# Kernel optimization log

Hardware: AMD Instinct MI355X
Metric: run time of the kernel (lower is better)

The kernel has to match this reference:

```python
import jax, jax.numpy as jnp
import numpy as np

H = 256
VOCAB = 32000
B = 128
T = 2048


def setup_inputs() -> dict:
    key = jax.random.key(0)
    ks = jax.random.split(key, 14)
    s = 0.05
    return {
        "tokens": jax.random.randint(ks[0], (B, 1), 0, VOCAB),
        "hidden": jax.random.normal(ks[1], (1, B, H), jnp.float32),
        "encoder_outputs": jax.random.normal(ks[2], (T, B, H), jnp.float32),
        "emb_table": jax.random.normal(ks[3], (VOCAB + 1, H), jnp.float32) * s,
        "attn_W": jax.random.normal(ks[4], (1, 2 * H), jnp.float32) * s,
        "attn_b": jax.random.normal(ks[5], (1,), jnp.float32) * s,
        "comb_W": jax.random.normal(ks[6], (H, 2 * H), jnp.float32) * s,
        "comb_b": jax.random.normal(ks[7], (H,), jnp.float32) * s,
        "gru_Wih": jax.random.normal(ks[8], (3 * H, H), jnp.float32) * s,
        "gru_Whh": jax.random.normal(ks[9], (3 * H, H), jnp.float32) * s,
        "gru_bih": jax.random.normal(ks[10], (3 * H,), jnp.float32) * s,
        "gru_bhh": jax.random.normal(ks[11], (3 * H,), jnp.float32) * s,
        "out_W": jax.random.normal(ks[12], (VOCAB, H), jnp.float32) * s,
        "out_b": jax.random.normal(ks[13], (VOCAB,), jnp.float32) * s,
    }


def reference(tokens, hidden, encoder_outputs, emb_table, attn_W, attn_b,
              comb_W, comb_b, gru_Wih, gru_Whh, gru_bih, gru_bhh, out_W, out_b):
    h = hidden.shape[-1]
    # Embedding lookup: [B,1] -> [B,1,H] -> [1,B,H]
    emb = jnp.transpose(emb_table[tokens], (1, 0, 2))
    # Additive attention: Linear([hidden; enc_t]) -> scalar score per position.
    # attn_W splits into hidden part (first H cols) and encoder part (last H).
    W_h, W_e = attn_W[:, :h], attn_W[:, h:]          # [1,H] each
    scores = (jnp.einsum('tbh,oh->tbo', encoder_outputs, W_e)
              + jnp.einsum('lbh,oh->lbo', hidden, W_h)  # broadcast over T
              + attn_b)                                  # [T,B,1]
    attn_w = jax.nn.softmax(scores, axis=0)              # softmax over time
    # Context: weighted sum over time -> [1,B,H]
    ctx = jnp.einsum('tbo,tbh->obh', attn_w, encoder_outputs)
    # Combine embedded input with context, relu
    x = jnp.concatenate([emb, ctx], axis=2)              # [1,B,2H]
    x = jax.nn.relu(jnp.einsum('lbk,hk->lbh', x, comb_W) + comb_b)  # [1,B,H]
    # Single GRU step (PyTorch gate ordering: r, z, n)
    gx = x[0] @ gru_Wih.T + gru_bih                      # [B,3H]
    gh = hidden[0] @ gru_Whh.T + gru_bhh                 # [B,3H]
    r = jax.nn.sigmoid(gx[:, :h] + gh[:, :h])
    z = jax.nn.sigmoid(gx[:, h:2 * h] + gh[:, h:2 * h])
    n = jnp.tanh(gx[:, 2 * h:] + r * gh[:, 2 * h:])
    h_new = ((1.0 - z) * n + z * hidden[0])[None]        # [1,B,H]
    # Output projection + log_softmax over vocab
    logits = jnp.einsum('lbh,vh->lbv', h_new, out_W) + out_b
    logp = jax.nn.log_softmax(logits, axis=2)            # [1,B,V]
    return (logp, h_new, jnp.transpose(attn_w, (1, 0, 2)), ctx)
```

## Files before the change

### kernel.cpp

```cpp
#include <hip/hip_runtime.h>
#include <cstddef>

constexpr int H  = 256;
constexpr int Bb = 128;
constexpr int T  = 2048;
constexpr int V  = 32000;
constexpr int SPLITS = 16;
constexpr int TC = T / SPLITS;

__global__ __launch_bounds__(256) void k_attn(
    const float* __restrict__ enc, const float* __restrict__ hidden,
    const float* __restrict__ attn_W, const float* __restrict__ attn_b,
    float* __restrict__ scores, float* __restrict__ ctx_part) {
  const int b = blockIdx.y, chunk = blockIdx.x, tid = threadIdx.x;
  const int lane = tid & 63, wave = tid >> 6;
  __shared__ float red[16];
  __shared__ float hb_sh;

  const float we = attn_W[H + tid];
  const float wh = attn_W[tid];
  const float hv = hidden[b * H + tid];

  float p = wh * hv;
  #pragma unroll
  for (int off = 32; off; off >>= 1) p += __shfl_down(p, off);
  if (lane == 0) red[wave] = p;
  __syncthreads();
  if (tid == 0) hb_sh = red[0] + red[1] + red[2] + red[3] + attn_b[0];
  __syncthreads();
  const float hb = hb_sh;

  float acc = 0.f;
  const float* encb = enc + (size_t)chunk * TC * (Bb * H) + (size_t)b * H + tid;
  const int t0base = chunk * TC;

  for (int t = 0; t < TC; t += 4) {
    float e0 = encb[(size_t)(t + 0) * (Bb * H)];
    float e1 = encb[(size_t)(t + 1) * (Bb * H)];
    float e2 = encb[(size_t)(t + 2) * (Bb * H)];
    float e3 = encb[(size_t)(t + 3) * (Bb * H)];
    float p0 = e0 * we, p1 = e1 * we, p2 = e2 * we, p3 = e3 * we;
    #pragma unroll
    for (int off = 32; off; off >>= 1) {
      p0 += __shfl_down(p0, off);
      p1 += __shfl_down(p1, off);
      p2 += __shfl_down(p2, off);
      p3 += __shfl_down(p3, off);
    }
    __syncthreads();
    if (lane == 0) {
      red[wave * 4 + 0] = p0; red[wave * 4 + 1] = p1;
      red[wave * 4 + 2] = p2; red[wave * 4 + 3] = p3;
    }
    __syncthreads();
    float s0 = red[0] + red[4] + red[8]  + red[12] + hb;
    float s1 = red[1] + red[5] + red[9]  + red[13] + hb;
    float s2 = red[2] + red[6] + red[10] + red[14] + hb;
    float s3 = red[3] + red[7] + red[11] + red[15] + hb;
    float w0 = __expf(s0), w1 = __expf(s1), w2 = __expf(s2), w3 = __expf(s3);
    acc += w0 * e0 + w1 * e1 + w2 * e2 + w3 * e3;
    if (tid < 4) {
      float sv = (tid == 0) ? s0 : (tid == 1) ? s1 : (tid == 2) ? s2 : s3;
      scores[(size_t)b * T + t0base + t + tid] = sv;
    }
  }
  ctx_part[((size_t)b * SPLITS + chunk) * H + tid] = acc;
}

__global__ __launch_bounds__(256) void k_softmax_ctx(
    const float* __restrict__ scores, const float* __restrict__ ctx_part,
    float* __restrict__ attn_o, float* __restrict__ ctx_o) {
  const int b = blockIdx.x, tid = threadIdx.x;
  const int lane = tid & 63, wave = tid >> 6;
  __shared__ float red[4];
  __shared__ float m_sh, l_sh;

  const float* sb = scores + (size_t)b * T;
  float s[8];
  #pragma unroll
  for (int q = 0; q < 8; q++) s[q] = sb[tid + 256 * q];

  float mx = s[0];
  #pragma unroll
  for (int q = 1; q < 8; q++) mx = fmaxf(mx, s[q]);
  #pragma unroll
  for (int off = 32; off; off >>= 1) mx = fmaxf(mx, __shfl_down(mx, off));
  if (lane == 0) red[wave] = mx;
  __syncthreads();
  if (tid == 0) m_sh = fmaxf(fmaxf(red[0], red[1]), fmaxf(red[2], red[3]));
  __syncthreads();
  const float m = m_sh;

  float w[8];
  float ps = 0.f;
  #pragma unroll
  for (int q = 0; q < 8; q++) { w[q] = __expf(s[q] - m); ps += w[q]; }
  #pragma unroll
  for (int off = 32; off; off >>= 1) ps += __shfl_down(ps, off);
  __syncthreads();
  if (lane == 0) red[wave] = ps;
  __syncthreads();
  if (tid == 0) l_sh = red[0] + red[1] + red[2] + red[3];
  __syncthreads();
  const float inv = 1.f / l_sh;

  #pragma unroll
  for (int q = 0; q < 8; q++) attn_o[(size_t)b * T + tid + 256 * q] = w[q] * inv;

  float c = 0.f;
  #pragma unroll
  for (int si = 0; si < SPLITS; si++) c += ctx_part[((size_t)b * SPLITS + si) * H + tid];
  ctx_o[(size_t)b * H + tid] = c * __expf(-m) * inv;
}

__global__ __launch_bounds__(256) void k_comb_gru(
    const int* __restrict__ tokens, const float* __restrict__ hidden,
    const float* __restrict__ emb_table,
    const float* __restrict__ comb_W, const float* __restrict__ comb_b,
    const float* __restrict__ Wih, const float* __restrict__ Whh,
    const float* __restrict__ bih, const float* __restrict__ bhh,
    const float* __restrict__ ctx_o, float* __restrict__ hnew) {
  const int b = blockIdx.x, tid = threadIdx.x;
  __shared__ __align__(16) float x2[2 * H];
  __shared__ __align__(16) float hid[H];
  __shared__ __align__(16) float xs[H];

  const int tok = tokens[b];
  x2[tid]     = emb_table[(size_t)tok * H + tid];
  x2[H + tid] = ctx_o[(size_t)b * H + tid];
  hid[tid]    = hidden[(size_t)b * H + tid];
  __syncthreads();

  {
    const float4* wr = (const float4*)(comb_W + (size_t)tid * (2 * H));
    const float4* xr = (const float4*)x2;
    float a = 0.f;
    #pragma unroll 8
    for (int k = 0; k < (2 * H) / 4; k++) {
      float4 w = wr[k], x = xr[k];
      a += w.x * x.x + w.y * x.y + w.z * x.z + w.w * x.w;
    }
    a += comb_b[tid];
    xs[tid] = fmaxf(a, 0.f);
  }
  __syncthreads();

  auto dot256 = [](const float* __restrict__ row, const float* __restrict__ v) -> float {
    const float4* r4 = (const float4*)row;
    const float4* v4 = (const float4*)v;
    float a = 0.f;
    #pragma unroll 8
    for (int k = 0; k < H / 4; k++) {
      float4 w = r4[k], x = v4[k];
      a += w.x * x.x + w.y * x.y + w.z * x.z + w.w * x.w;
    }
    return a;
  };

  float gxr = dot256(Wih + (size_t)tid * H,             xs) + bih[tid];
  float gxz = dot256(Wih + (size_t)(tid + H) * H,       xs) + bih[tid + H];
  float gxn = dot256(Wih + (size_t)(tid + 2 * H) * H,   xs) + bih[tid + 2 * H];
  float ghr = dot256(Whh + (size_t)tid * H,             hid) + bhh[tid];
  float ghz = dot256(Whh + (size_t)(tid + H) * H,       hid) + bhh[tid + H];
  float ghn = dot256(Whh + (size_t)(tid + 2 * H) * H,   hid) + bhh[tid + 2 * H];

  float r = 1.f / (1.f + __expf(-(gxr + ghr)));
  float z = 1.f / (1.f + __expf(-(gxz + ghz)));
  float n = tanhf(gxn + r * ghn);
  hnew[(size_t)b * H + tid] = (1.f - z) * n + z * hid[tid];
}

__global__ __launch_bounds__(256) void k_logits(
    const float* __restrict__ hnew, const float* __restrict__ out_W,
    const float* __restrict__ out_b, float* __restrict__ logits) {
  const int tid = threadIdx.x;
  const int v0 = blockIdx.x * 128;
  const int tx = tid & 15, ty = tid >> 4;
  __shared__ __align__(16) float lW[128][36];
  __shared__ __align__(16) float lH[128][36];

  float acc[8][8];
  #pragma unroll
  for (int i = 0; i < 8; i++)
    #pragma unroll
    for (int j = 0; j < 8; j++) acc[i][j] = 0.f;

  for (int k0 = 0; k0 < H; k0 += 32) {
    #pragma unroll
    for (int q = 0; q < 4; q++) {
      int idx = q * 1024 + tid * 4;
      int r = idx >> 5, c = idx & 31;
      float4 wv = *(const float4*)(out_W + (size_t)(v0 + r) * H + k0 + c);
      *(float4*)(&lW[r][c]) = wv;
      float4 hv = *(const float4*)(hnew + (size_t)r * H + k0 + c);
      *(float4*)(&lH[r][c]) = hv;
    }
    __syncthreads();
    #pragma unroll 4
    for (int kk = 0; kk < 32; kk++) {
      float hreg[8], wreg[8];
      #pragma unroll
      for (int i = 0; i < 8; i++) hreg[i] = lH[ty + 16 * i][kk];
      #pragma unroll
      for (int j = 0; j < 8; j++) wreg[j] = lW[tx + 16 * j][kk];
      #pragma unroll
      for (int i = 0; i < 8; i++)
        #pragma unroll
        for (int j = 0; j < 8; j++)
          acc[i][j] = fmaf(hreg[i], wreg[j], acc[i][j]);
    }
    __syncthreads();
  }

  float bj[8];
  #pragma unroll
  for (int j = 0; j < 8; j++) bj[j] = out_b[v0 + tx + 16 * j];
  #pragma unroll
  for (int i = 0; i < 8; i++) {
    int b = ty + 16 * i;
    float* dst = logits + (size_t)b * V + v0 + tx;
    #pragma unroll
    for (int j = 0; j < 8; j++) dst[16 * j] = acc[i][j] + bj[j];
  }
}

__global__ __launch_bounds__(256) void k_lse(
    const float* __restrict__ logits, float* __restrict__ lse) {
  const int b = blockIdx.x, tid = threadIdx.x;
  const int lane = tid & 63, wave = tid >> 6;
  __shared__ float mred[4], lred[4];
  const float* lb = logits + (size_t)b * V;
  float m = -1e30f, l = 0.f;
  for (int v = tid; v < V; v += 256) {
    float x = lb[v];
    float nm = fmaxf(m, x);
    l = l * __expf(m - nm) + __expf(x - nm);
    m = nm;
  }
  #pragma unroll
  for (int off = 32; off; off >>= 1) {
    float mo = __shfl_down(m, off), lo = __shfl_down(l, off);
    float nm = fmaxf(m, mo);
    l = l * __expf(m - nm) + lo * __expf(mo - nm);
    m = nm;
  }
  if (lane == 0) { mred[wave] = m; lred[wave] = l; }
  __syncthreads();
  if (tid == 0) {
    float M = mred[0], L = lred[0];
    #pragma unroll
    for (int w = 1; w < 4; w++) {
      float nm = fmaxf(M, mred[w]);
      L = L * __expf(M - nm) + lred[w] * __expf(mred[w] - nm);
      M = nm;
    }
    lse[b] = M + logf(L);
  }
}

__global__ __launch_bounds__(256) void k_sub(
    float* __restrict__ logits, const float* __restrict__ lse) {
  const int v = blockIdx.x * 256 + threadIdx.x;
  const int b = blockIdx.y;
  logits[(size_t)b * V + v] -= lse[b];
}

extern "C" void kernel_launch(void* const* d_in, const int* in_sizes, int n_in,
                              void* d_out, int out_size, void* d_ws, size_t ws_size,
                              hipStream_t stream) {
  const int*   tokens = (const int*)d_in[0];
  const float* hidden = (const float*)d_in[1];
  const float* enc    = (const float*)d_in[2];
  const float* emb    = (const float*)d_in[3];
  const float* attn_W = (const float*)d_in[4];
  const float* attn_b = (const float*)d_in[5];
  const float* comb_W = (const float*)d_in[6];
  const float* comb_b = (const float*)d_in[7];
  const float* Wih    = (const float*)d_in[8];
  const float* Whh    = (const float*)d_in[9];
  const float* bih    = (const float*)d_in[10];
  const float* bhh    = (const float*)d_in[11];
  const float* out_W  = (const float*)d_in[12];
  const float* out_b  = (const float*)d_in[13];

  float* out    = (float*)d_out;
  float* logp   = out;
  float* hnew   = out + (size_t)Bb * V;
  float* attn_o = hnew + (size_t)Bb * H;
  float* ctx_o  = attn_o + (size_t)Bb * T;

  float* ws       = (float*)d_ws;
  float* scores   = ws;
  float* ctx_part = ws + (size_t)Bb * T;
  float* lse      = ctx_part + (size_t)Bb * SPLITS * H;

  k_attn<<<dim3(SPLITS, Bb), 256, 0, stream>>>(enc, hidden, attn_W, attn_b, scores, ctx_part);
  k_softmax_ctx<<<dim3(Bb), 256, 0, stream>>>(scores, ctx_part, attn_o, ctx_o);
  k_comb_gru<<<dim3(Bb), 256, 0, stream>>>(tokens, hidden, emb, comb_W, comb_b,
                                           Wih, Whh, bih, bhh, ctx_o, hnew);
  k_logits<<<dim3(V / 128), 256, 0, stream>>>(hnew, out_W, out_b, logp);
  k_lse<<<dim3(Bb), 256, 0, stream>>>(logp, lse);
  k_sub<<<dim3(V / 256, Bb), 256, 0, stream>>>(logp, lse);
}
```

Baseline: 585.8 us.

## Use bf16 MFMA for vocab projection, per-wave attention, split LSE, vectorize

The vocab projection now converts hidden state and out_W to bf16 and computes logits with MFMA 16x16x32 instructions instead of scalar FP32 FMAs. The attention kernel gives each wave its own slice of time with float4 loads and wave-only reductions, which removes the per-step block barriers at the cost of four times as many context partials. The LSE reduction is split across four blocks per row and the subtract pass is vectorized. bf16 rounding of the logit inputs trades some precision for matrix-core throughput.

```diff
diff --git a/kernel.cpp b/kernel.cpp
--- a/kernel.cpp
+++ b/kernel.cpp
@@ -7,64 +7,77 @@
 constexpr int V  = 32000;
 constexpr int SPLITS = 16;
 constexpr int TC = T / SPLITS;
+constexpr int NPART = SPLITS * 4;
+constexpr int LSE_SPLIT = 4;
+constexpr int VS = V / LSE_SPLIT;
+
+typedef __attribute__((ext_vector_type(8))) short short8;
+typedef __attribute__((ext_vector_type(4))) float f32x4;
+
+__device__ __forceinline__ unsigned short bf1(float a) {
+  unsigned u = __builtin_bit_cast(unsigned, a);
+  return (unsigned short)((u + 0x7fffu + ((u >> 16) & 1u)) >> 16);
+}
+__device__ __forceinline__ unsigned bfpack2(float a, float b) {
+  unsigned ua = __builtin_bit_cast(unsigned, a);
+  unsigned ub = __builtin_bit_cast(unsigned, b);
+  ua = (ua + 0x7fffu + ((ua >> 16) & 1u)) >> 16;
+  ub = (ub + 0x7fffu + ((ub >> 16) & 1u)) & 0xffff0000u;
+  return ua | ub;
+}
 
 __global__ __launch_bounds__(256) void k_attn(
     const float* __restrict__ enc, const float* __restrict__ hidden,
     const float* __restrict__ attn_W, const float* __restrict__ attn_b,
     float* __restrict__ scores, float* __restrict__ ctx_part) {
-  const int b = blockIdx.y, chunk = blockIdx.x, tid = threadIdx.x;
-  const int lane = tid & 63, wave = tid >> 6;
-  __shared__ float red[16];
-  __shared__ float hb_sh;
-
-  const float we = attn_W[H + tid];
-  const float wh = attn_W[tid];
-  const float hv = hidden[b * H + tid];
-
-  float p = wh * hv;
-  #pragma unroll
-  for (int off = 32; off; off >>= 1) p += __shfl_down(p, off);
-  if (lane == 0) red[wave] = p;
-  __syncthreads();
-  if (tid == 0) hb_sh = red[0] + red[1] + red[2] + red[3] + attn_b[0];
-  __syncthreads();
-  const float hb = hb_sh;
-
-  float acc = 0.f;
-  const float* encb = enc + (size_t)chunk * TC * (Bb * H) + (size_t)b * H + tid;
-  const int t0base = chunk * TC;
-
-  for (int t = 0; t < TC; t += 4) {
-    float e0 = encb[(size_t)(t + 0) * (Bb * H)];
-    float e1 = encb[(size_t)(t + 1) * (Bb * H)];
-    float e2 = encb[(size_t)(t + 2) * (Bb * H)];
-    float e3 = encb[(size_t)(t + 3) * (Bb * H)];
-    float p0 = e0 * we, p1 = e1 * we, p2 = e2 * we, p3 = e3 * we;
-    #pragma unroll
-    for (int off = 32; off; off >>= 1) {
-      p0 += __shfl_down(p0, off);
-      p1 += __shfl_down(p1, off);
-      p2 += __shfl_down(p2, off);
-      p3 += __shfl_down(p3, off);
-    }
-    __syncthreads();
+  const int b = blockIdx.y, chunk = blockIdx.x;
+  const int tid = threadIdx.x, lane = tid & 63, wave = tid >> 6;
+
+  const float4 we = *(const float4*)(attn_W + H + lane * 4);
+  const float4 wh = *(const float4*)(attn_W + lane * 4);
+  const float4 hv = *(const float4*)(hidden + (size_t)b * H + lane * 4);
+
+  float hb = fmaf(wh.x, hv.x, fmaf(wh.y, hv.y, fmaf(wh.z, hv.z, wh.w * hv.w)));
+  #pragma unroll
+  for (int off = 1; off < 64; off <<= 1) hb += __shfl_xor(hb, off);
+  hb += attn_b[0];
+
+  const int t0 = chunk * TC + wave * 32;
+  const float* base = enc + (size_t)t0 * (Bb * H) + (size_t)b * H + lane * 4;
+
+  float4 acc = {0.f, 0.f, 0.f, 0.f};
+  for (int i = 0; i < 32; i += 4) {
+    float4 e0 = *(const float4*)(base + (size_t)(i + 0) * (Bb * H));
+    float4 e1 = *(const float4*)(base + (size_t)(i + 1) * (Bb * H));
+    float4 e2 = *(const float4*)(base + (size_t)(i + 2) * (Bb * H));
+    float4 e3 = *(const float4*)(base + (size_t)(i + 3) * (Bb * H));
+
+    float p0 = fmaf(e0.x, we.x, fmaf(e0.y, we.y, fmaf(e0.z, we.z, e0.w * we.w)));
+    float p1 = fmaf(e1.x, we.x, fmaf(e1.y, we.y, fmaf(e1.z, we.z, e1.w * we.w)));
+    float p2 = fmaf(e2.x, we.x, fmaf(e2.y, we.y, fmaf(e2.z, we.z, e2.w * we.w)));
+    float p3 = fmaf(e3.x, we.x, fmaf(e3.y, we.y, fmaf(e3.z, we.z, e3.w * we.w)));
+    #pragma unroll
+    for (int off = 1; off < 64; off <<= 1) {
+      p0 += __shfl_xor(p0, off);
+      p1 += __shfl_xor(p1, off);
+      p2 += __shfl_xor(p2, off);
+      p3 += __shfl_xor(p3, off);
+    }
+    float s0 = p0 + hb, s1 = p1 + hb, s2 = p2 + hb, s3 = p3 + hb;
+    float w0 = __expf(s0), w1 = __expf(s1), w2 = __expf(s2), w3 = __expf(s3);
+
+    acc.x = fmaf(w0, e0.x, fmaf(w1, e1.x, fmaf(w2, e2.x, fmaf(w3, e3.x, acc.x))));
+    acc.y = fmaf(w0, e0.y, fmaf(w1, e1.y, fmaf(w2, e2.y, fmaf(w3, e3.y, acc.y))));
+    acc.z = fmaf(w0, e0.z, fmaf(w1, e1.z, fmaf(w2, e2.z, fmaf(w3, e3.z, acc.z))));
+    acc.w = fmaf(w0, e0.w, fmaf(w1, e1.w, fmaf(w2, e2.w, fmaf(w3, e3.w, acc.w))));
+
     if (lane == 0) {
-      red[wave * 4 + 0] = p0; red[wave * 4 + 1] = p1;
-      red[wave * 4 + 2] = p2; red[wave * 4 + 3] = p3;
-    }
-    __syncthreads();
-    float s0 = red[0] + red[4] + red[8]  + red[12] + hb;
-    float s1 = red[1] + red[5] + red[9]  + red[13] + hb;
-    float s2 = red[2] + red[6] + red[10] + red[14] + hb;
-    float s3 = red[3] + red[7] + red[11] + red[15] + hb;
-    float w0 = __expf(s0), w1 = __expf(s1), w2 = __expf(s2), w3 = __expf(s3);
-    acc += w0 * e0 + w1 * e1 + w2 * e2 + w3 * e3;
-    if (tid < 4) {
-      float sv = (tid == 0) ? s0 : (tid == 1) ? s1 : (tid == 2) ? s2 : s3;
-      scores[(size_t)b * T + t0base + t + tid] = sv;
-    }
-  }
-  ctx_part[((size_t)b * SPLITS + chunk) * H + tid] = acc;
+      float4 sv = {s0, s1, s2, s3};
+      *(float4*)(scores + (size_t)b * T + t0 + i) = sv;
+    }
+  }
+  float* cp = ctx_part + ((size_t)b * NPART + chunk * 4 + wave) * H + lane * 4;
+  *(float4*)cp = acc;
 }
 
 __global__ __launch_bounds__(256) void k_softmax_ctx(
@@ -84,7 +97,7 @@
   #pragma unroll
   for (int q = 1; q < 8; q++) mx = fmaxf(mx, s[q]);
   #pragma unroll
-  for (int off = 32; off; off >>= 1) mx = fmaxf(mx, __shfl_down(mx, off));
+  for (int off = 1; off < 64; off <<= 1) mx = fmaxf(mx, __shfl_xor(mx, off));
   if (lane == 0) red[wave] = mx;
   __syncthreads();
   if (tid == 0) m_sh = fmaxf(fmaxf(red[0], red[1]), fmaxf(red[2], red[3]));
@@ -96,7 +109,7 @@
   #pragma unroll
   for (int q = 0; q < 8; q++) { w[q] = __expf(s[q] - m); ps += w[q]; }
   #pragma unroll
-  for (int off = 32; off; off >>= 1) ps += __shfl_down(ps, off);
+  for (int off = 1; off < 64; off <<= 1) ps += __shfl_xor(ps, off);
   __syncthreads();
   if (lane == 0) red[wave] = ps;
   __syncthreads();
@@ -108,8 +121,8 @@
   for (int q = 0; q < 8; q++) attn_o[(size_t)b * T + tid + 256 * q] = w[q] * inv;
 
   float c = 0.f;
-  #pragma unroll
-  for (int si = 0; si < SPLITS; si++) c += ctx_part[((size_t)b * SPLITS + si) * H + tid];
+  for (int si = 0; si < NPART; si++)
+    c += ctx_part[((size_t)b * NPART + si) * H + tid];
   ctx_o[(size_t)b * H + tid] = c * __expf(-m) * inv;
 }
 
@@ -119,7 +132,8 @@
     const float* __restrict__ comb_W, const float* __restrict__ comb_b,
     const float* __restrict__ Wih, const float* __restrict__ Whh,
     const float* __restrict__ bih, const float* __restrict__ bhh,
-    const float* __restrict__ ctx_o, float* __restrict__ hnew) {
+    const float* __restrict__ ctx_o, float* __restrict__ hnew,
+    unsigned short* __restrict__ hnewb) {
   const int b = blockIdx.x, tid = threadIdx.x;
   __shared__ __align__(16) float x2[2 * H];
   __shared__ __align__(16) float hid[H];
@@ -157,112 +171,148 @@
     return a;
   };
 
-  float gxr = dot256(Wih + (size_t)tid * H,             xs) + bih[tid];
-  float gxz = dot256(Wih + (size_t)(tid + H) * H,       xs) + bih[tid + H];
-  float gxn = dot256(Wih + (size_t)(tid + 2 * H) * H,   xs) + bih[tid + 2 * H];
-  float ghr = dot256(Whh + (size_t)tid * H,             hid) + bhh[tid];
-  float ghz = dot256(Whh + (size_t)(tid + H) * H,       hid) + bhh[tid + H];
-  float ghn = dot256(Whh + (size_t)(tid + 2 * H) * H,   hid) + bhh[tid + 2 * H];
+  float gxr = dot256(Wih + (size_t)tid * H,           xs) + bih[tid];
+  float gxz = dot256(Wih + (size_t)(tid + H) * H,     xs) + bih[tid + H];
+  float gxn = dot256(Wih + (size_t)(tid + 2 * H) * H, xs) + bih[tid + 2 * H];
+  float ghr = dot256(Whh + (size_t)tid * H,           hid) + bhh[tid];
+  float ghz = dot256(Whh + (size_t)(tid + H) * H,     hid) + bhh[tid + H];
+  float ghn = dot256(Whh + (size_t)(tid + 2 * H) * H, hid) + bhh[tid + 2 * H];
 
   float r = 1.f / (1.f + __expf(-(gxr + ghr)));
   float z = 1.f / (1.f + __expf(-(gxz + ghz)));
   float n = tanhf(gxn + r * ghn);
-  hnew[(size_t)b * H + tid] = (1.f - z) * n + z * hid[tid];
-}
-
+  float hv = (1.f - z) * n + z * hid[tid];
+  hnew[(size_t)b * H + tid] = hv;
+  hnewb[(size_t)b * H + tid] = bf1(hv);
+}
+
+constexpr int LSTR = 72;
 __global__ __launch_bounds__(256) void k_logits(
-    const float* __restrict__ hnew, const float* __restrict__ out_W,
+    const unsigned short* __restrict__ hnewb, const float* __restrict__ out_W,
     const float* __restrict__ out_b, float* __restrict__ logits) {
   const int tid = threadIdx.x;
+  const int lane = tid & 63, wave = tid >> 6;
   const int v0 = blockIdx.x * 128;
-  const int tx = tid & 15, ty = tid >> 4;
-  __shared__ __align__(16) float lW[128][36];
-  __shared__ __align__(16) float lH[128][36];
-
-  float acc[8][8];
-  #pragma unroll
-  for (int i = 0; i < 8; i++)
-    #pragma unroll
-    for (int j = 0; j < 8; j++) acc[i][j] = 0.f;
-
-  for (int k0 = 0; k0 < H; k0 += 32) {
+  const int r16 = lane & 15, quad = lane >> 4;
+
+  __shared__ __align__(16) short lA[128 * LSTR];
+  __shared__ __align__(16) short lB[128 * LSTR];
+
+  f32x4 acc[8][2];
+  #pragma unroll
+  for (int mt = 0; mt < 8; mt++) {
+    acc[mt][0] = (f32x4){0.f, 0.f, 0.f, 0.f};
+    acc[mt][1] = (f32x4){0.f, 0.f, 0.f, 0.f};
+  }
+
+  for (int k0 = 0; k0 < H; k0 += 64) {
     #pragma unroll
     for (int q = 0; q < 4; q++) {
-      int idx = q * 1024 + tid * 4;
-      int r = idx >> 5, c = idx & 31;
-      float4 wv = *(const float4*)(out_W + (size_t)(v0 + r) * H + k0 + c);
-      *(float4*)(&lW[r][c]) = wv;
-      float4 hv = *(const float4*)(hnew + (size_t)r * H + k0 + c);
-      *(float4*)(&lH[r][c]) = hv;
+      int idx = q * 256 + tid;
+      int row = idx >> 3, c8 = idx & 7;
+      f32x4 v = *(const f32x4*)(hnewb + (size_t)row * H + k0 + c8 * 8);
+      *(f32x4*)(&lA[row * LSTR + c8 * 8]) = v;
+    }
+    #pragma unroll
+    for (int q = 0; q < 8; q++) {
+      int idx = q * 256 + tid;
+      int row = idx >> 4, c4 = idx & 15;
+      f32x4 wv = *(const f32x4*)(out_W + (size_t)(v0 + row) * H + k0 + c4 * 4);
+      uint2 p;
+      p.x = bfpack2(wv.x, wv.y);
+      p.y = bfpack2(wv.z, wv.w);
+      *(uint2*)(&lB[row * LSTR + c4 * 4]) = p;
     }
     __syncthreads();
-    #pragma unroll 4
-    for (int kk = 0; kk < 32; kk++) {
-      float hreg[8], wreg[8];
+    #pragma unroll
+    for (int ks = 0; ks < 2; ks++) {
+      short8 bf[2];
       #pragma unroll
-      for (int i = 0; i < 8; i++) hreg[i] = lH[ty + 16 * i][kk];
+      for (int nt = 0; nt < 2; nt++) {
+        int row = wave * 32 + nt * 16 + r16;
+        bf[nt] = *(const short8*)(&lB[row * LSTR + ks * 32 + quad * 8]);
+      }
       #pragma unroll
-      for (int j = 0; j < 8; j++) wreg[j] = lW[tx + 16 * j][kk];
+      for (int mt = 0; mt < 8; mt++) {
+        short8 af = *(const short8*)(&lA[(mt * 16 + r16) * LSTR + ks * 32 + quad * 8]);
+        acc[mt][0] = __builtin_amdgcn_mfma_f32_16x16x32_bf16(af, bf[0], acc[mt][0], 0, 0, 0);
+        acc[mt][1] = __builtin_amdgcn_mfma_f32_16x16x32_bf16(af, bf[1], acc[mt][1], 0, 0, 0);
+      }
+    }
+    __syncthreads();
+  }
+
+  #pragma unroll
+  for (int nt = 0; nt < 2; nt++) {
+    int col = v0 + wave * 32 + nt * 16 + r16;
+    float bias = out_b[col];
+    #pragma unroll
+    for (int mt = 0; mt < 8; mt++) {
+      int brow = mt * 16 + quad * 4;
       #pragma unroll
-      for (int i = 0; i < 8; i++)
-        #pragma unroll
-        for (int j = 0; j < 8; j++)
-          acc[i][j] = fmaf(hreg[i], wreg[j], acc[i][j]);
-    }
-    __syncthreads();
-  }
-
-  float bj[8];
-  #pragma unroll
-  for (int j = 0; j < 8; j++) bj[j] = out_b[v0 + tx + 16 * j];
-  #pragma unroll
-  for (int i = 0; i < 8; i++) {
-    int b = ty + 16 * i;
-    float* dst = logits + (size_t)b * V + v0 + tx;
-    #pragma unroll
-    for (int j = 0; j < 8; j++) dst[16 * j] = acc[i][j] + bj[j];
+      for (int r = 0; r < 4; r++)
+        logits[(size_t)(brow + r) * V + col] = acc[mt][nt][r] + bias;
+    }
   }
 }
 
 __global__ __launch_bounds__(256) void k_lse(
-    const float* __restrict__ logits, float* __restrict__ lse) {
-  const int b = blockIdx.x, tid = threadIdx.x;
+    const float* __restrict__ logits, float2* __restrict__ lse_part) {
+  const int b = blockIdx.x, s = blockIdx.y, tid = threadIdx.x;
   const int lane = tid & 63, wave = tid >> 6;
-  __shared__ float mred[4], lred[4];
-  const float* lb = logits + (size_t)b * V;
-  float m = -1e30f, l = 0.f;
-  for (int v = tid; v < V; v += 256) {
-    float x = lb[v];
-    float nm = fmaxf(m, x);
-    l = l * __expf(m - nm) + __expf(x - nm);
-    m = nm;
-  }
-  #pragma unroll
-  for (int off = 32; off; off >>= 1) {
-    float mo = __shfl_down(m, off), lo = __shfl_down(l, off);
+  const float4* base = (const float4*)(logits + (size_t)b * V + (size_t)s * VS);
+
+  float4 m4 = {-1e30f, -1e30f, -1e30f, -1e30f};
+  float4 l4 = {0.f, 0.f, 0.f, 0.f};
+  for (int i = tid; i < VS / 4; i += 256) {
+    float4 x = base[i];
+    float nm;
+    nm = fmaxf(m4.x, x.x); l4.x = l4.x * __expf(m4.x - nm) + __expf(x.x - nm); m4.x = nm;
+    nm = fmaxf(m4.y, x.y); l4.y = l4.y * __expf(m4.y - nm) + __expf(x.y - nm); m4.y = nm;
+    nm = fmaxf(m4.z, x.z); l4.z = l4.z * __expf(m4.z - nm) + __expf(x.z - nm); m4.z = nm;
+    nm = fmaxf(m4.w, x.w); l4.w = l4.w * __expf(m4.w - nm) + __expf(x.w - nm); m4.w = nm;
+  }
+  float m = fmaxf(fmaxf(m4.x, m4.y), fmaxf(m4.z, m4.w));
+  float l = l4.x * __expf(m4.x - m) + l4.y * __expf(m4.y - m) +
+            l4.z * __expf(m4.z - m) + l4.w * __expf(m4.w - m);
+  #pragma unroll
+  for (int off = 1; off < 64; off <<= 1) {
+    float mo = __shfl_xor(m, off), lo = __shfl_xor(l, off);
     float nm = fmaxf(m, mo);
     l = l * __expf(m - nm) + lo * __expf(mo - nm);
     m = nm;
   }
-  if (lane == 0) { mred[wave] = m; lred[wave] = l; }
+  __shared__ float sm[4], sl[4];
+  if (lane == 0) { sm[wave] = m; sl[wave] = l; }
   __syncthreads();
   if (tid == 0) {
-    float M = mred[0], L = lred[0];
-    #pragma unroll
-    for (int w = 1; w < 4; w++) {
-      float nm = fmaxf(M, mred[w]);
-      L = L * __expf(M - nm) + lred[w] * __expf(mred[w] - nm);
+    float M = sm[0], L = sl[0];
+    #pragma unroll
+    for (int w2 = 1; w2 < 4; w2++) {
+      float nm = fmaxf(M, sm[w2]);
+      L = L * __expf(M - nm) + sl[w2] * __expf(sm[w2] - nm);
       M = nm;
     }
-    lse[b] = M + logf(L);
+    lse_part[b * LSE_SPLIT + s] = make_float2(M, L);
   }
 }
 
 __global__ __launch_bounds__(256) void k_sub(
-    float* __restrict__ logits, const float* __restrict__ lse) {
-  const int v = blockIdx.x * 256 + threadIdx.x;
+    float* __restrict__ logits, const float2* __restrict__ lse_part) {
   const int b = blockIdx.y;
-  logits[(size_t)b * V + v] -= lse[b];
+  const int i = blockIdx.x * 256 + threadIdx.x;
+  float2 p0 = lse_part[b * 4 + 0], p1 = lse_part[b * 4 + 1];
+  float2 p2 = lse_part[b * 4 + 2], p3 = lse_part[b * 4 + 3];
+  float M = fmaxf(fmaxf(p0.x, p1.x), fmaxf(p2.x, p3.x));
+  float L = p0.y * __expf(p0.x - M) + p1.y * __expf(p1.x - M) +
+            p2.y * __expf(p2.x - M) + p3.y * __expf(p3.x - M);
+  float lse = M + logf(L);
+  if (i < V / 4) {
+    float4* p = (float4*)(logits + (size_t)b * V) + i;
+    float4 x = *p;
+    x.x -= lse; x.y -= lse; x.z -= lse; x.w -= lse;
+    *p = x;
+  }
 }
 
 extern "C" void kernel_launch(void* const* d_in, const int* in_sizes, int n_in,
@@ -292,13 +342,14 @@
   float* ws       = (float*)d_ws;
   float* scores   = ws;
   float* ctx_part = ws + (size_t)Bb * T;
-  float* lse      = ctx_part + (size_t)Bb * SPLITS * H;
+  float2* lse_part = (float2*)(ctx_part + (size_t)Bb * NPART * H);
+  unsigned short* hnewb = (unsigned short*)(lse_part + Bb * LSE_SPLIT);
 
   k_attn<<<dim3(SPLITS, Bb), 256, 0, stream>>>(enc, hidden, attn_W, attn_b, scores, ctx_part);
   k_softmax_ctx<<<dim3(Bb), 256, 0, stream>>>(scores, ctx_part, attn_o, ctx_o);
   k_comb_gru<<<dim3(Bb), 256, 0, stream>>>(tokens, hidden, emb, comb_W, comb_b,
-                                           Wih, Whh, bih, bhh, ctx_o, hnew);
-  k_logits<<<dim3(V / 128), 256, 0, stream>>>(hnew, out_W, out_b, logp);
-  k_lse<<<dim3(Bb), 256, 0, stream>>>(logp, lse);
-  k_sub<<<dim3(V / 256, Bb), 256, 0, stream>>>(logp, lse);
-}
+                                           Wih, Whh, bih, bhh, ctx_o, hnew, hnewb);
+  k_logits<<<dim3(V / 128), 256, 0, stream>>>(hnewb, out_W, out_b, logp);
+  k_lse<<<dim3(Bb, LSE_SPLIT), 256, 0, stream>>>(logp, lse_part);
+  k_sub<<<dim3(V / 1024 + 1, Bb), 256, 0, stream>>>(logp, lse_part);
+}
```

Result: faster. 508.5 us (-13.2%).
